# Optimization experiments

Measured on AMD Instinct MI355X. Metric: run time of the kernel, lower is better.

Reference implementation:

```python
import jax, jax.numpy as jnp
import numpy as np

BATCH = 65536
INPUT_DIM = 128
NUM_KNOTS = 10
DEGREE = 3  # n_basis = NUM_KNOTS - DEGREE - 1 = 6


def bspline_basis(x, knots, degree):
    """Cox-de Boor B-spline basis, vectorized over all batch/feature entries.

    x: [B, D] (already clipped into [knots[0], knots[-1]))
    knots: [K] uniform knot vector
    returns: [B, D, K - degree - 1]
    """
    xe = x[..., None]                                            # [B, D, 1]
    # degree-0 indicator basis: [B, D, K-1]
    B = ((xe >= knots[:-1]) & (xe < knots[1:])).astype(x.dtype)
    for d in range(1, degree + 1):
        left_den = knots[d:-1] - knots[:-(d + 1)]                # [K-1-d]
        right_den = knots[d + 1:] - knots[1:-d]                  # [K-1-d]
        safe_l = jnp.where(left_den > 0, left_den, 1.0)
        safe_r = jnp.where(right_den > 0, right_den, 1.0)
        left = jnp.where(left_den > 0, (xe - knots[:-(d + 1)]) / safe_l, 0.0) * B[..., :-1]
        right = jnp.where(right_den > 0, (knots[d + 1:] - xe) / safe_r, 0.0) * B[..., 1:]
        B = left + right                                          # [B, D, K-1-d]
    return B


def setup_inputs() -> dict:
    key = jax.random.key(0)
    k1, k2 = jax.random.split(key)
    x = jax.random.normal(k1, (BATCH, INPUT_DIM), dtype=jnp.float32)
    interaction_weights = jax.random.normal(k2, (INPUT_DIM, INPUT_DIM), dtype=jnp.float32)
    return {"x": x, "interaction_weights": interaction_weights}


def reference(x, interaction_weights):
    # Shared uniform knot vector over [-1, 1], identical across all features
    knots = jnp.linspace(-1.0, 1.0, NUM_KNOTS).astype(x.dtype)
    eps = 1e-6
    xc = jnp.clip(x, knots[0], knots[-1] - eps)
    basis = bspline_basis(xc, knots, DEGREE)                     # [B, D, 6]
    B_sz = x.shape[0]
    basis_flat = basis.reshape(B_sz, -1)                         # [B, D*6]
    # interaction: out[b, j] = sum_i x[b,i]^2 * sigmoid(W[i,j])
    # (equivalent to bmm(x^T, x * sigmoid(W)) in the original, without
    #  materializing the [B, D, D] broadcast intermediate)
    S = jax.nn.sigmoid(interaction_weights)                      # [D, D]
    interaction = (x * x) @ S                                    # [B, D]
    return jnp.concatenate([basis_flat, interaction], axis=1)    # [B, D*6 + D]
```

## Files before the change

### kernel.cpp

```cpp
#include <hip/hip_runtime.h>
#include <math.h>

#define BATCH 65536
#define DIM 128
#define NBAS 6
#define OUTW 896
#define ROWS_PER_TILE 32
#define CHROWS 8
#define NCHUNK 4
#define XT_F 128
#define BAS_F 768

typedef float f4v __attribute__((ext_vector_type(4)));
typedef float f32x4 __attribute__((ext_vector_type(4)));
typedef _Float16 f16x4 __attribute__((ext_vector_type(4)));
typedef _Float16 f16x8 __attribute__((ext_vector_type(8)));

__global__ __launch_bounds__(256) void sigmoid_kT(const float* __restrict__ W,
                                                  _Float16* __restrict__ ST) {
    int t = blockIdx.x * 256 + threadIdx.x;
    int i = t >> 7;
    int j = t & 127;
    float w = W[t];
    float s = 1.0f / (1.0f + expf(-w));
    ST[j * 128 + i] = (_Float16)s;
}

__device__ __forceinline__ void bw(float x, int& s,
                                   float& w0, float& w1, float& w2, float& w3) {
    const float i6 = 0.16666666666666666f;
    float xc = fminf(fmaxf(x, -1.0f), 1.0f - 1e-6f);
    float p  = (xc + 1.0f) * 4.5f;
    float sf = floorf(p);
    float u  = p - sf;
    s = (int)sf;
    float u2 = u * u;
    float v  = 1.0f - u;
    w0 = u * u2 * i6;
    w1 = (((-3.0f * u + 3.0f) * u + 3.0f) * u + 1.0f) * i6;
    w2 = ((3.0f * u - 6.0f) * u2 + 4.0f) * i6;
    w3 = v * v * v * i6;
}

__global__ __launch_bounds__(256, 3) void kan_main(const float* __restrict__ X,
                                                   const _Float16* __restrict__ ST,
                                                   float* __restrict__ out) {
    __shared__ __align__(16) float xTf[ROWS_PER_TILE * XT_F];
    __shared__ __align__(16) _Float16 xsq[ROWS_PER_TILE * 128];
    __shared__ __align__(16) float bas[CHROWS * BAS_F];

    const int tid = threadIdx.x;
    const int row0 = blockIdx.x * ROWS_PER_TILE;

    const float4* X4 = (const float4*)(X + (size_t)row0 * DIM);
    float4* xT4 = (float4*)xTf;
#pragma unroll
    for (int k = 0; k < 4; ++k) {
        int e4 = k * 256 + tid;
        int r = e4 >> 5;
        int i4 = e4 & 31;
        float4 xv = X4[e4];
        xT4[e4] = xv;
        f16x4 q = {(_Float16)(xv.x * xv.x), (_Float16)(xv.y * xv.y),
                   (_Float16)(xv.z * xv.z), (_Float16)(xv.w * xv.w)};
        int byte = (r * 256 + i4 * 8) ^ ((r & 7) << 4);
        *(f16x4*)((char*)xsq + byte) = q;
    }
    f4v z4 = {0.0f, 0.0f, 0.0f, 0.0f};
    f4v* bas4 = (f4v*)bas;
#pragma unroll
    for (int k = 0; k < 6; ++k) bas4[k * 256 + tid] = z4;
    __syncthreads();

    {
        const int w = tid >> 6, l = tid & 63;
        const int lr = l & 15, lg = l >> 4;
        const int rt = w & 1;
        const int ch = w >> 1;

        f16x8 af[4];
#pragma unroll
        for (int kk = 0; kk < 4; ++kk) {
            int byte = ((rt * 16 + lr) * 256 + kk * 64 + lg * 16) ^ ((lr & 7) << 4);
            af[kk] = *(const f16x8*)((const char*)xsq + byte);
        }

        f32x4 acc[4];
#pragma unroll
        for (int ct = 0; ct < 4; ++ct) acc[ct] = (f32x4){0.f, 0.f, 0.f, 0.f};

        const char* stb = (const char*)ST;
#pragma unroll
        for (int ct = 0; ct < 4; ++ct) {
            const char* bp = stb + (ch * 64 + ct * 16 + lr) * 256 + lg * 16;
#pragma unroll
            for (int kk = 0; kk < 4; ++kk) {
                f16x8 bf = *(const f16x8*)(bp + kk * 64);
                acc[ct] = __builtin_amdgcn_mfma_f32_16x16x32_f16(af[kk], bf, acc[ct], 0, 0, 0);
            }
        }

#pragma unroll
        for (int ct = 0; ct < 4; ++ct) {
            int colb = ch * 64 + ct * 16 + lr;
#pragma unroll
            for (int q = 0; q < 4; ++q) {
                int rowi = rt * 16 + lg * 4 + q;
                __builtin_nontemporal_store(
                    acc[ct][q],
                    out + (size_t)(row0 + rowi) * OUTW + DIM * NBAS + colb);
            }
        }
    }

    {
        const int sr = tid >> 5;
        const int f0 = tid & 31;
        for (int c = 0; c < NCHUNK; ++c) {
            const float* xrow = xTf + (c * CHROWS + sr) * XT_F;
            float* basr = bas + sr * BAS_F;
#pragma unroll
            for (int m = 0; m < 4; ++m) {
                int f = f0 + 32 * m;
                float x = xrow[f];
                int s;
                float w0, w1, w2, w3;
                bw(x, s, w0, w1, w2, w3);
                float* bp = basr + f * NBAS + s;
                if (s <= 5)           bp[0]  = w0;
                if (s >= 1 && s <= 6) bp[-1] = w1;
                if (s >= 2 && s <= 7) bp[-2] = w2;
                if (s >= 3)           bp[-3] = w3;
            }
            __syncthreads();

            float* ob = out + (size_t)(row0 + c * CHROWS) * OUTW;
#pragma unroll
            for (int k = 0; k < 6; ++k) {
                int idx = k * 256 + tid;
                int r = idx / 192;
                int j = idx - r * 192;
                f4v v = bas4[idx];
                __builtin_nontemporal_store(v, (f4v*)(ob + (size_t)r * OUTW + 4 * j));
                bas4[idx] = z4;
            }
            __syncthreads();
        }
    }
}

extern "C" void kernel_launch(void* const* d_in, const int* in_sizes, int n_in,
                              void* d_out, int out_size, void* d_ws, size_t ws_size,
                              hipStream_t stream) {
    const float* X = (const float*)d_in[0];
    const float* W = (const float*)d_in[1];
    float* out = (float*)d_out;
    _Float16* ST = (_Float16*)d_ws;

    sigmoid_kT<<<(DIM * DIM) / 256, 256, 0, stream>>>(W, ST);
    kan_main<<<BATCH / ROWS_PER_TILE, 256, 0, stream>>>(X, ST, out);
}
```

Before: 269.8 us.

## Split fused kernel into separate GEMM and basis kernels

Result: no change. 270.9 us (+0.4%).

```diff
diff --git a/kernel.cpp b/kernel.cpp
--- a/kernel.cpp
+++ b/kernel.cpp
@@ -5,15 +5,11 @@
 #define DIM 128
 #define NBAS 6
 #define OUTW 896
-#define ROWS_PER_TILE 32
 #define CHROWS 8
-#define NCHUNK 4
-#define XT_F 128
 #define BAS_F 768
 
 typedef float f4v __attribute__((ext_vector_type(4)));
 typedef float f32x4 __attribute__((ext_vector_type(4)));
-typedef _Float16 f16x4 __attribute__((ext_vector_type(4)));
 typedef _Float16 f16x8 __attribute__((ext_vector_type(8)));
 
 __global__ __launch_bounds__(256) void sigmoid_kT(const float* __restrict__ W,
@@ -24,6 +20,57 @@
     float w = W[t];
     float s = 1.0f / (1.0f + expf(-w));
     ST[j * 128 + i] = (_Float16)s;
+}
+
+__global__ __launch_bounds__(256) void gemm_k(const float* __restrict__ X,
+                                              const _Float16* __restrict__ ST,
+                                              float* __restrict__ out) {
+    const int tid = threadIdx.x;
+    const int w = tid >> 6, l = tid & 63;
+    const int lr = l & 15, lg = l >> 4;
+    const int rt = w & 1;
+    const int ch = w >> 1;
+    const int rowA = blockIdx.x * 32 + rt * 16 + lr;
+
+    const float4* xr = (const float4*)(X + (size_t)rowA * DIM);
+    f16x8 af[4];
+#pragma unroll
+    for (int kk = 0; kk < 4; ++kk) {
+        float4 a = xr[kk * 8 + lg * 2 + 0];
+        float4 b = xr[kk * 8 + lg * 2 + 1];
+        f16x8 v = {(_Float16)(a.x * a.x), (_Float16)(a.y * a.y),
+                   (_Float16)(a.z * a.z), (_Float16)(a.w * a.w),
+                   (_Float16)(b.x * b.x), (_Float16)(b.y * b.y),
+                   (_Float16)(b.z * b.z), (_Float16)(b.w * b.w)};
+        af[kk] = v;
+    }
+
+    f32x4 acc[4];
+#pragma unroll
+    for (int ct = 0; ct < 4; ++ct) acc[ct] = (f32x4){0.f, 0.f, 0.f, 0.f};
+
+    const char* stb = (const char*)ST;
+#pragma unroll
+    for (int ct = 0; ct < 4; ++ct) {
+        const char* bp = stb + (ch * 64 + ct * 16 + lr) * 256 + lg * 16;
+#pragma unroll
+        for (int kk = 0; kk < 4; ++kk) {
+            f16x8 bf = *(const f16x8*)(bp + kk * 64);
+            acc[ct] = __builtin_amdgcn_mfma_f32_16x16x32_f16(af[kk], bf, acc[ct], 0, 0, 0);
+        }
+    }
+
+    const int rowC0 = blockIdx.x * 32 + rt * 16 + lg * 4;
+#pragma unroll
+    for (int ct = 0; ct < 4; ++ct) {
+        int colb = ch * 64 + ct * 16 + lr;
+#pragma unroll
+        for (int q = 0; q < 4; ++q) {
+            __builtin_nontemporal_store(
+                acc[ct][q],
+                out + (size_t)(rowC0 + q) * OUTW + DIM * NBAS + colb);
+        }
+    }
 }
 
 __device__ __forceinline__ void bw(float x, int& s,
@@ -42,110 +89,46 @@
     w3 = v * v * v * i6;
 }
 
-__global__ __launch_bounds__(256, 3) void kan_main(const float* __restrict__ X,
-                                                   const _Float16* __restrict__ ST,
-                                                   float* __restrict__ out) {
-    __shared__ __align__(16) float xTf[ROWS_PER_TILE * XT_F];
-    __shared__ __align__(16) _Float16 xsq[ROWS_PER_TILE * 128];
+__global__ __launch_bounds__(256, 6) void basis_k(const float* __restrict__ X,
+                                                  float* __restrict__ out) {
     __shared__ __align__(16) float bas[CHROWS * BAS_F];
+    f4v* bas4 = (f4v*)bas;
 
     const int tid = threadIdx.x;
-    const int row0 = blockIdx.x * ROWS_PER_TILE;
+    const int row0 = blockIdx.x * CHROWS;
 
-    const float4* X4 = (const float4*)(X + (size_t)row0 * DIM);
-    float4* xT4 = (float4*)xTf;
-#pragma unroll
-    for (int k = 0; k < 4; ++k) {
-        int e4 = k * 256 + tid;
-        int r = e4 >> 5;
-        int i4 = e4 & 31;
-        float4 xv = X4[e4];
-        xT4[e4] = xv;
-        f16x4 q = {(_Float16)(xv.x * xv.x), (_Float16)(xv.y * xv.y),
-                   (_Float16)(xv.z * xv.z), (_Float16)(xv.w * xv.w)};
-        int byte = (r * 256 + i4 * 8) ^ ((r & 7) << 4);
-        *(f16x4*)((char*)xsq + byte) = q;
-    }
     f4v z4 = {0.0f, 0.0f, 0.0f, 0.0f};
-    f4v* bas4 = (f4v*)bas;
 #pragma unroll
     for (int k = 0; k < 6; ++k) bas4[k * 256 + tid] = z4;
     __syncthreads();
 
-    {
-        const int w = tid >> 6, l = tid & 63;
-        const int lr = l & 15, lg = l >> 4;
-        const int rt = w & 1;
-        const int ch = w >> 1;
+    const int sr = tid >> 5;
+    const int f0 = tid & 31;
+    const float* xrow = X + (size_t)(row0 + sr) * DIM;
+    float* basr = bas + sr * BAS_F;
+#pragma unroll
+    for (int m = 0; m < 4; ++m) {
+        int f = f0 + 32 * m;
+        float x = xrow[f];
+        int s;
+        float w0, w1, w2, w3;
+        bw(x, s, w0, w1, w2, w3);
+        float* bp = basr + f * NBAS + s;
+        if (s <= 5)           bp[0]  = w0;
+        if (s >= 1 && s <= 6) bp[-1] = w1;
+        if (s >= 2 && s <= 7) bp[-2] = w2;
+        if (s >= 3)           bp[-3] = w3;
+    }
+    __syncthreads();
 
-        f16x8 af[4];
+    float* ob = out + (size_t)row0 * OUTW;
 #pragma unroll
-        for (int kk = 0; kk < 4; ++kk) {
-            int byte = ((rt * 16 + lr) * 256 + kk * 64 + lg * 16) ^ ((lr & 7) << 4);
-            af[kk] = *(const f16x8*)((const char*)xsq + byte);
-        }
-
-        f32x4 acc[4];
-#pragma unroll
-        for (int ct = 0; ct < 4; ++ct) acc[ct] = (f32x4){0.f, 0.f, 0.f, 0.f};
-
-        const char* stb = (const char*)ST;
-#pragma unroll
-        for (int ct = 0; ct < 4; ++ct) {
-            const char* bp = stb + (ch * 64 + ct * 16 + lr) * 256 + lg * 16;
-#pragma unroll
-            for (int kk = 0; kk < 4; ++kk) {
-                f16x8 bf = *(const f16x8*)(bp + kk * 64);
-                acc[ct] = __builtin_amdgcn_mfma_f32_16x16x32_f16(af[kk], bf, acc[ct], 0, 0, 0);
-            }
-        }
-
-#pragma unroll
-        for (int ct = 0; ct < 4; ++ct) {
-            int colb = ch * 64 + ct * 16 + lr;
-#pragma unroll
-            for (int q = 0; q < 4; ++q) {
-                int rowi = rt * 16 + lg * 4 + q;
-                __builtin_nontemporal_store(
-                    acc[ct][q],
-                    out + (size_t)(row0 + rowi) * OUTW + DIM * NBAS + colb);
-            }
-        }
-    }
-
-    {
-        const int sr = tid >> 5;
-        const int f0 = tid & 31;
-        for (int c = 0; c < NCHUNK; ++c) {
-            const float* xrow = xTf + (c * CHROWS + sr) * XT_F;
-            float* basr = bas + sr * BAS_F;
-#pragma unroll
-            for (int m = 0; m < 4; ++m) {
-                int f = f0 + 32 * m;
-                float x = xrow[f];
-                int s;
-                float w0, w1, w2, w3;
-                bw(x, s, w0, w1, w2, w3);
-                float* bp = basr + f * NBAS + s;
-                if (s <= 5)           bp[0]  = w0;
-                if (s >= 1 && s <= 6) bp[-1] = w1;
-                if (s >= 2 && s <= 7) bp[-2] = w2;
-                if (s >= 3)           bp[-3] = w3;
-            }
-            __syncthreads();
-
-            float* ob = out + (size_t)(row0 + c * CHROWS) * OUTW;
-#pragma unroll
-            for (int k = 0; k < 6; ++k) {
-                int idx = k * 256 + tid;
-                int r = idx / 192;
-                int j = idx - r * 192;
-                f4v v = bas4[idx];
-                __builtin_nontemporal_store(v, (f4v*)(ob + (size_t)r * OUTW + 4 * j));
-                bas4[idx] = z4;
-            }
-            __syncthreads();
-        }
+    for (int k = 0; k < 6; ++k) {
+        int idx = k * 256 + tid;
+        int r = idx / 192;
+        int j = idx - r * 192;
+        f4v v = bas4[idx];
+        __builtin_nontemporal_store(v, (f4v*)(ob + (size_t)r * OUTW + 4 * j));
     }
 }
 
@@ -158,5 +141,6 @@
     _Float16* ST = (_Float16*)d_ws;
 
     sigmoid_kT<<<(DIM * DIM) / 256, 256, 0, stream>>>(W, ST);
-    kan_main<<<BATCH / ROWS_PER_TILE, 256, 0, stream>>>(X, ST, out);
+    gemm_k<<<BATCH / 32, 256, 0, stream>>>(X, ST, out);
+    basis_k<<<BATCH / CHROWS, 256, 0, stream>>>(X, out);
 }
```
